# Kernel optimization log

Hardware: AMD Instinct MI355X
Metric: run time of the kernel (lower is better)

The kernel has to match this reference:

```python
import jax, jax.numpy as jnp
import numpy as np
import math

B, N, D = 2, 192, 256

def _linear_params(key, d_in, d_out):
    kw, kb = jax.random.split(key)
    scale = 1.0 / math.sqrt(d_in)
    W = jax.random.uniform(kw, (d_out, d_in), jnp.float32, -scale, scale)
    b = jax.random.uniform(kb, (d_out,), jnp.float32, -scale, scale)
    return W, b

def setup_inputs() -> dict:
    key = jax.random.key(0)
    ks = jax.random.split(key, 7)
    Edges = jax.random.normal(ks[0], (B, N * N, D), jnp.float32)
    Wq_w, Wq_b = _linear_params(ks[1], D, D)
    Wk_w, Wk_b = _linear_params(ks[2], D, D)
    Wv_w, Wv_b = _linear_params(ks[3], D, D)
    Wb_w, Wb_b = _linear_params(ks[4], D, 1)
    Wg_w, Wg_b = _linear_params(ks[5], D, D)
    Wo_w, Wo_b = _linear_params(ks[6], D, D)
    return {"Edges": Edges, "Wq_w": Wq_w, "Wq_b": Wq_b, "Wk_w": Wk_w, "Wk_b": Wk_b,
            "Wv_w": Wv_w, "Wv_b": Wv_b, "Wb_w": Wb_w, "Wb_b": Wb_b,
            "Wg_w": Wg_w, "Wg_b": Wg_b, "Wo_w": Wo_w, "Wo_b": Wo_b}

def reference(Edges, Wq_w, Wq_b, Wk_w, Wk_b, Wv_w, Wv_b, Wb_w, Wb_b, Wg_w, Wg_b, Wo_w, Wo_b):
    # Edges: [B, N*N, D]; dropout is identity in eval mode.
    Bb, NN, Dd = Edges.shape
    n = int(round(math.sqrt(NN)))
    q = (Edges @ Wq_w.T + Wq_b).reshape(Bb, n, n, Dd)
    k = (Edges @ Wk_w.T + Wk_b).reshape(Bb, n, n, Dd)
    v = (Edges @ Wv_w.T + Wv_b).reshape(Bb, n, n, Dd)
    bmat = (Edges @ Wb_w.T + Wb_b).reshape(Bb, n, n)          # b[b,i,l]
    g = jax.nn.sigmoid(Edges @ Wg_w.T + Wg_b)                  # [B, N*N, D]
    # row attention: q(i,j) . k(i,l) ; column attention: q(i,j) . k(l,j)
    scores = (jnp.einsum('bijd,bild->bijl', q, k)
              + jnp.einsum('bijd,bljd->bijl', q, k)) / math.sqrt(Dd)
    sym_bias = bmat + jnp.swapaxes(bmat, 1, 2)                 # b[i,l] + b[l,i]
    alpha = jax.nn.softmax(scores + sym_bias[:, :, None, :], axis=-1)  # [B,n,n,n]
    # first value contraction along rows; second term matches torch's
    # transpose-free add: out2[b,i,j,d] = sum_l alpha[b,j,i,l] v[b,l,i,d]
    o1 = jnp.einsum('bijl,bild->bijd', alpha, v)
    o2 = jnp.einsum('bjil,blid->bijd', alpha, v)
    out = g * (o1 + o2).reshape(Bb, NN, Dd)
    out = jax.nn.relu(out @ Wo_w.T + Wo_b)
    return out
```

## Files before the change

kernel.cpp:

```cpp
#include <hip/hip_runtime.h>
#include <hip/hip_bf16.h>

typedef __hip_bfloat16 bf16;
typedef unsigned short u16;
typedef __attribute__((ext_vector_type(8))) short bf16x8;
typedef __attribute__((ext_vector_type(4))) float f32x4;

#define NB   2
#define NG   192
#define DD   256
#define NN2  (NG*NG)
#define MT   (NB*NN2)

static __device__ __forceinline__ float bfu2f(u16 u){
    return __uint_as_float(((unsigned)u) << 16);
}
static __device__ __forceinline__ u16 f2bfu(float f){
    bf16 h = __float2bfloat16(f);
    return *(u16*)&h;
}

static __device__ __forceinline__ void gl_lds16(const void* g, void* l){
    __builtin_amdgcn_global_load_lds(
        (const __attribute__((address_space(1))) unsigned int*)g,
        (__attribute__((address_space(3))) unsigned int*)l, 16, 0, 0);
}
static __device__ __forceinline__ int swz3(int x){ return ((x ^ (x>>3)) & 7) << 3; }

__global__ __launch_bounds__(256) void k_cast_eb(
    const float* __restrict__ E, const float* __restrict__ Wb,
    const float* __restrict__ bb, u16* __restrict__ Eb, float* __restrict__ bm)
{
    const int t = threadIdx.x;
    size_t base = (size_t)blockIdx.x*2048 + t*8;
    float4 x = *(const float4*)(E+base);
    float4 y = *(const float4*)(E+base+4);
    ushort4 a; a.x=f2bfu(x.x); a.y=f2bfu(x.y); a.z=f2bfu(x.z); a.w=f2bfu(x.w);
    ushort4 b; b.x=f2bfu(y.x); b.y=f2bfu(y.y); b.z=f2bfu(y.z); b.w=f2bfu(y.w);
    *(ushort4*)(Eb+base)   = a;
    *(ushort4*)(Eb+base+4) = b;
    const int l32 = t & 31;
    float4 w0 = ((const float4*)Wb)[l32*2];
    float4 w1 = ((const float4*)Wb)[l32*2+1];
    float s = x.x*w0.x + x.y*w0.y + x.z*w0.z + x.w*w0.w
            + y.x*w1.x + y.y*w1.y + y.z*w1.z + y.w*w1.w;
    #pragma unroll
    for (int off=1; off<32; off<<=1) s += __shfl_xor(s, off);
    if (l32 == 0) bm[blockIdx.x*8 + (t>>5)] = s + bb[0];
}

__global__ __launch_bounds__(256) void k_cast_w(
    const float* __restrict__ Wq, const float* __restrict__ Wk,
    const float* __restrict__ Wv, const float* __restrict__ Wg,
    const float* __restrict__ Wo,
    const float* __restrict__ bq, const float* __restrict__ bk,
    const float* __restrict__ bv, const float* __restrict__ bg,
    u16* __restrict__ Wcat, u16* __restrict__ Wob, float* __restrict__ biascat)
{
    int e = blockIdx.x*256 + threadIdx.x;
    Wcat[e]          = f2bfu(Wq[e]);
    Wcat[65536 + e]  = f2bfu(Wk[e]);
    Wcat[131072 + e] = f2bfu(Wv[e]);
    Wcat[196608 + e] = f2bfu(Wg[e]);
    Wob[e]           = f2bfu(Wo[e]);
    if (e < 1024){
        int p = e>>8, r = e&255;
        const float* bp = p==0?bq : p==1?bk : p==2?bv : bg;
        biascat[e] = bp[r];
    }
}

__global__ __launch_bounds__(256) void k_bias_sym(
    const float* __restrict__ bm, float* __restrict__ biassym)
{
    int rem = blockIdx.x*256 + threadIdx.x;
    int b = blockIdx.y;
    int i = rem / NG, l = rem % NG;
    biassym[(size_t)b*NN2 + rem] = bm[(size_t)b*NN2 + rem] + bm[(size_t)b*NN2 + l*NG + i];
}

static __device__ __forceinline__ void gemm128_dbuf(
    const u16* __restrict__ A, const u16* __restrict__ B,
    u16* As, u16* Bs, f32x4 acc[4][4], int t)
{
    const int lane = t & 63, w = t >> 6;
    const int wm = (w>>1)*64, wn = (w&1)*64;
    int offA[4], offB[4];
    #pragma unroll
    for (int f=0; f<4; f++){
        int ra = wm + f*16 + (lane&15);
        offA[f] = ra*32 + (((lane>>4) ^ ((ra>>1)&3)) << 3);
        int rb = wn + f*16 + (lane&15);
        offB[f] = rb*32 + (((lane>>4) ^ ((rb>>1)&3)) << 3);
    }
    auto stage = [&](int buf, int k0){
        #pragma unroll
        for (int it=0; it<2; it++){
            int c = it*256 + t;
            int row = c >> 2;
            int ks  = (c&3) ^ ((row>>1)&3);
            gl_lds16(A + (size_t)row*DD + k0 + ks*8, As + buf*4096 + c*8);
            gl_lds16(B + (size_t)row*DD + k0 + ks*8, Bs + buf*4096 + c*8);
        }
    };
    stage(0, 0);
    for (int ks=0; ks<8; ks++){
        if (ks<7){
            stage((ks+1)&1, (ks+1)*32);
            asm volatile("s_waitcnt vmcnt(4)" ::: "memory");
        } else {
            asm volatile("s_waitcnt vmcnt(0)" ::: "memory");
        }
        __builtin_amdgcn_s_barrier();
        const u16* Ab = As + (ks&1)*4096;
        const u16* Bb = Bs + (ks&1)*4096;
        bf16x8 a[4], b[4];
        #pragma unroll
        for (int f=0; f<4; f++) a[f] = *(const bf16x8*)(Ab + offA[f]);
        #pragma unroll
        for (int f=0; f<4; f++) b[f] = *(const bf16x8*)(Bb + offB[f]);
        #pragma unroll
        for (int mf=0; mf<4; mf++)
            #pragma unroll
            for (int nf=0; nf<4; nf++)
                acc[mf][nf] = __builtin_amdgcn_mfma_f32_16x16x32_bf16(a[mf], b[nf], acc[mf][nf], 0, 0, 0);
        __builtin_amdgcn_s_barrier();
    }
}

__global__ __launch_bounds__(256) void k_proj_mfma(
    const u16* __restrict__ Eb, const u16* __restrict__ Wcat,
    const float* __restrict__ biascat,
    u16* __restrict__ qb, u16* __restrict__ kb,
    u16* __restrict__ vb, u16* __restrict__ gb)
{
    __shared__ u16 As[2*4096];
    __shared__ u16 Bs[2*4096];
    const int blk = blockIdx.x;
    const int xj = blk & 7, xi = blk >> 3;
    const int m0 = (xj*72 + (xi>>3)) * 128;
    const int n0 = (xi & 7) * 128;
    const int t = threadIdx.x, lane = t&63, w = t>>6;
    f32x4 acc[4][4];
    #pragma unroll
    for (int i=0;i<4;i++)
        #pragma unroll
        for (int j=0;j<4;j++) acc[i][j] = f32x4{0.f,0.f,0.f,0.f};
    gemm128_dbuf(Eb + (size_t)m0*DD, Wcat + (size_t)n0*DD, As, Bs, acc, t);

    const int p = n0 >> 8;
    u16* outp = p==0?qb : p==1?kb : p==2?vb : gb;
    const int wm = (w>>1)*64, wn = (w&1)*64;
    #pragma unroll
    for (int mf=0; mf<4; mf++){
        int m = m0 + wm + mf*16 + (lane>>4)*4;
        #pragma unroll
        for (int nf=0; nf<4; nf++){
            int gn = n0 + wn + nf*16 + (lane&15);
            float bias = biascat[gn];
            int col = gn & 255;
            #pragma unroll
            for (int r=0; r<4; r++){
                float v = acc[mf][nf][r] + bias;
                if (p==3) v = 1.0f/(1.0f+__expf(-v));
                outp[(size_t)(m+r)*DD + col] = f2bfu(v);
            }
        }
    }
}

__global__ __launch_bounds__(256) void k_final_mfma(
    const u16* __restrict__ hb, const u16* __restrict__ Wob,
    const float* __restrict__ bo, float* __restrict__ out)
{
    __shared__ u16 As[2*4096];
    __shared__ u16 Bs[2*4096];
    const int blk = blockIdx.x;
    const int xj = blk & 7, xi = blk >> 3;
    const int m0 = (xj*72 + (xi>>1)) * 128;
    const int n0 = (xi & 1) * 128;
    const int t = threadIdx.x, lane = t&63, w = t>>6;
    f32x4 acc[4][4];
    #pragma unroll
    for (int i=0;i<4;i++)
        #pragma unroll
        for (int j=0;j<4;j++) acc[i][j] = f32x4{0.f,0.f,0.f,0.f};
    gemm128_dbuf(hb + (size_t)m0*DD, Wob + (size_t)n0*DD, As, Bs, acc, t);

    const int wm = (w>>1)*64, wn = (w&1)*64;
    #pragma unroll
    for (int mf=0; mf<4; mf++){
        int m = m0 + wm + mf*16 + (lane>>4)*4;
        #pragma unroll
        for (int nf=0; nf<4; nf++){
            int n = n0 + wn + nf*16 + (lane&15);
            float bias = bo[n];
            #pragma unroll
            for (int r=0; r<4; r++)
                out[(size_t)(m+r)*DD + n] = fmaxf(acc[mf][nf][r] + bias, 0.0f);
        }
    }
}

__global__ __launch_bounds__(512, 2) void k_scores(
    const u16* __restrict__ q, const u16* __restrict__ kmat,
    u16* __restrict__ S1, u16* __restrict__ S2T)
{
    __shared__ u16 As[2][NG*64];
    __shared__ u16 Bs[2][NG*64];
    const int MODE = blockIdx.y;
    const int z = blockIdx.x, b = z/NG, r = z%NG;
    const int t = threadIdx.x, lane = t&63, w = t>>6;
    const int wm = (w&3)*48, wn = (w>>2)*96;
    const size_t astr = MODE ? (size_t)NG*DD : (size_t)DD;
    const u16* Ab = MODE ? q    + ((size_t)b*NN2 + r)*DD : q    + ((size_t)b*NG + r)*NG*DD;
    const u16* Bb = MODE ? kmat + ((size_t)b*NN2 + r)*DD : kmat + ((size_t)b*NG + r)*NG*DD;

    f32x4 acc[3][6];
    #pragma unroll
    for (int i=0;i<3;i++)
        #pragma unroll
        for (int j=0;j<6;j++) acc[i][j] = f32x4{0.f,0.f,0.f,0.f};

    int offA[3], offB[6];
    #pragma unroll
    for (int mf=0; mf<3; mf++){
        int x = wm + mf*16 + (lane&15);
        offA[mf] = x*64 + (((lane>>4)<<3) ^ swz3(x));
    }
    #pragma unroll
    for (int nf=0; nf<6; nf++){
        int x = wn + nf*16 + (lane&15);
        offB[nf] = x*64 + (((lane>>4)<<3) ^ swz3(x));
    }

    auto stage = [&](int buf, int k0){
        #pragma unroll
        for (int rr=0; rr<3; rr++){
            int c = t + rr*512;
            int x = c>>3, l8e = (c&7)<<3;
            size_t ro = (size_t)x*astr + k0;
            gl_lds16(Ab + ro + (l8e ^ swz3(x)), &As[buf][c*8]);
            gl_lds16(Bb + ro + (l8e ^ swz3(x)), &Bs[buf][c*8]);
        }
    };

    stage(0, 0);
    for (int ks=0; ks<4; ks++){
        if (ks<3){
            stage((ks+1)&1, (ks+1)*64);
            asm volatile("s_waitcnt vmcnt(6)" ::: "memory");
        } else {
            asm volatile("s_waitcnt vmcnt(0)" ::: "memory");
        }
        __builtin_amdgcn_s_barrier();
        const u16* A = &As[ks&1][0];
        const u16* B = &Bs[ks&1][0];
        #pragma unroll
        for (int kk=0; kk<2; kk++){
            bf16x8 a[3];
            #pragma unroll
            for (int mf=0; mf<3; mf++) a[mf] = *(const bf16x8*)(A + (offA[mf]^(kk<<5)));
            #pragma unroll
            for (int nf=0; nf<6; nf++){
                bf16x8 bf = *(const bf16x8*)(B + (offB[nf]^(kk<<5)));
                #pragma unroll
                for (int mf=0; mf<3; mf++)
                    acc[mf][nf] = __builtin_amdgcn_mfma_f32_16x16x32_bf16(a[mf], bf, acc[mf][nf], 0, 0, 0);
            }
        }
        __builtin_amdgcn_s_barrier();
    }

    u16* outb = (MODE ? S2T : S1) + ((size_t)b*NG + r)*NN2;
    #pragma unroll
    for (int mf=0; mf<3; mf++){
        #pragma unroll
        for (int nf=0; nf<6; nf++){
            int lcol = wn + nf*16 + (lane&15);
            #pragma unroll
            for (int r4=0; r4<4; r4++){
                int x = wm + mf*16 + (lane>>4)*4 + r4;
                outb[(size_t)x*NG + lcol] = f2bfu(acc[mf][nf][r4]*0.0625f);
            }
        }
    }
}

__global__ __launch_bounds__(256) void k_softmax(
    const u16* __restrict__ S1, const u16* __restrict__ S2T,
    const float* __restrict__ biassym,
    u16* __restrict__ alpha, u16* __restrict__ alphaT)
{
    int rr   = blockIdx.x*4 + (threadIdx.x >> 6);
    int lane = threadIdx.x & 63;
    int b = blockIdx.y;
    int i = rr / NG, j = rr % NG;
    const u16* r1 = S1  + ((size_t)b*NN2 + rr)*NG;
    const u16* r2 = S2T + ((size_t)b*NN2 + (size_t)j*NG + i)*NG;
    const float* bs = biassym + ((size_t)b*NG + i)*NG;
    float vals[3];
    float mx = -1e30f;
    #pragma unroll
    for (int tt=0; tt<3; tt++){
        int l = lane + tt*64;
        float s = bfu2f(r1[l]) + bfu2f(r2[l]) + bs[l];
        vals[tt] = s;
        mx = fmaxf(mx, s);
    }
    #pragma unroll
    for (int off=32; off; off>>=1) mx = fmaxf(mx, __shfl_xor(mx, off));
    float sum = 0.f;
    #pragma unroll
    for (int tt=0; tt<3; tt++){ vals[tt] = __expf(vals[tt]-mx); sum += vals[tt]; }
    #pragma unroll
    for (int off=32; off; off>>=1) sum += __shfl_xor(sum, off);
    float inv = 1.0f/sum;
    u16* arow1 = alpha  + ((size_t)b*NN2 + rr)*NG;
    u16* arow2 = alphaT + ((size_t)b*NN2 + (size_t)j*NG + i)*NG;
    #pragma unroll
    for (int tt=0; tt<3; tt++){
        u16 vq = f2bfu(vals[tt]*inv);
        arow1[lane + tt*64] = vq;
        arow2[lane + tt*64] = vq;
    }
}

__global__ __launch_bounds__(512, 4) void k_attnout(
    const u16* __restrict__ alpha, const u16* __restrict__ alphaT,
    const u16* __restrict__ vb, const u16* __restrict__ gb, u16* __restrict__ hb)
{
    __shared__ u16 AsL[2][NG*64];
    __shared__ u16 Vs[128*64];
    const int z = blockIdx.x;
    const int xcd = z & 7, s = z >> 3;
    const int bi = xcd*48 + (s>>1), dh = s & 1;
    const int b = bi/NG, i = bi%NG;
    const int dbase = dh*128;
    const int t = threadIdx.x, lane = t&63, w = t>>6;
    const int wm = (w&1)*96, wn = (w>>1)*32;

    const u16* Abase0 = alpha  + (size_t)bi*NN2;
    const u16* Abase1 = alphaT + (size_t)bi*NN2;
    const u16* V0 = vb + (size_t)bi*NG*DD + dbase;
    const u16* V1 = vb + ((size_t)b*NG*NG + i)*DD + dbase;

    f32x4 acc[6][2];
    #pragma unroll
    for (int m=0;m<6;m++)
        #pragma unroll
        for (int n=0;n<2;n++) acc[m][n] = f32x4{0.f,0.f,0.f,0.f};

    int offA[6], offB[2];
    #pragma unroll
    for (int mf=0; mf<6; mf++){
        int j = wm + mf*16 + (lane&15);
        offA[mf] = j*64 + (((lane>>4)<<3) ^ swz3(j));
    }
    #pragma unroll
    for (int nf=0; nf<2; nf++){
        int d = wn + nf*16 + (lane&15);
        offB[nf] = d*64 + (((lane>>4)<<3) ^ swz3(d));
    }

    int4 vr[2];
    auto stageA = [&](int u, int buf){
        const u16* Ab = (u>=3) ? Abase1 : Abase0;
        int ls = (u>=3 ? u-3 : u)*64;
        #pragma unroll
        for (int rr=0; rr<3; rr++){
            int c = t + rr*512;
            int j = c>>3, l8e = (c&7)<<3;
            gl_lds16(Ab + (size_t)j*NG + ls + (l8e ^ swz3(j)), &AsL[buf][c*8]);
        }
    };
    auto loadV = [&](int u){
        int p = (u>=3), ls = (u>=3 ? u-3 : u)*64;
        #pragma unroll
        for (int rr=0; rr<2; rr++){
            int c = t + rr*512;
            int l = ls + (c>>4), d0 = (c&15)*8;
            const u16* src = p ? (V1 + (size_t)l*NG*DD + d0) : (V0 + (size_t)l*DD + d0);
            vr[rr] = *(const int4*)src;
        }
    };

    stageA(0, 0);
    loadV(0);
    for (int u=0; u<6; u++){
        #pragma unroll
        for (int rr=0; rr<2; rr++){
            int c = t + rr*512;
            int l = c>>4;
            l &= 63;
            int d0 = (c&15)*8, c3 = c&7;
            ushort* vp = (ushort*)&vr[rr];
            #pragma unroll
            for (int qd=0; qd<8; qd++)
                Vs[(d0+qd)*64 + (l ^ ((qd^c3)<<3))] = vp[qd];
        }
        if (u<5){ stageA(u+1, (u+1)&1); loadV(u+1); }
        asm volatile("s_waitcnt lgkmcnt(0)" ::: "memory");
        __builtin_amdgcn_s_barrier();
        const u16* A = &AsL[u&1][0];
        #pragma unroll
        for (int kk=0; kk<2; kk++){
            bf16x8 bfr[2];
            #pragma unroll
            for (int nf=0; nf<2; nf++) bfr[nf] = *(const bf16x8*)(Vs + (offB[nf]^(kk<<5)));
            #pragma unroll
            for (int mf=0; mf<6; mf++){
                bf16x8 afr = *(const bf16x8*)(A + (offA[mf]^(kk<<5)));
                acc[mf][0] = __builtin_amdgcn_mfma_f32_16x16x32_bf16(afr, bfr[0], acc[mf][0], 0, 0, 0);
                acc[mf][1] = __builtin_amdgcn_mfma_f32_16x16x32_bf16(afr, bfr[1], acc[mf][1], 0, 0, 0);
            }
        }
        __builtin_amdgcn_s_barrier();
    }

    #pragma unroll
    for (int mf=0; mf<6; mf++){
        #pragma unroll
        for (int nf=0; nf<2; nf++){
            #pragma unroll
            for (int r4=0; r4<4; r4++){
                int j = wm + mf*16 + (lane>>4)*4 + r4;
                int d = dbase + wn + nf*16 + (lane&15);
                size_t idx = ((size_t)bi*NG + j)*DD + d;
                hb[idx] = f2bfu(bfu2f(gb[idx]) * acc[mf][nf][r4]);
            }
        }
    }
}

extern "C" void kernel_launch(void* const* d_in, const int* in_sizes, int n_in,
                              void* d_out, int out_size, void* d_ws, size_t ws_size,
                              hipStream_t stream)
{
    const float* E  = (const float*)d_in[0];
    const float* Wq = (const float*)d_in[1];  const float* bq = (const float*)d_in[2];
    const float* Wk = (const float*)d_in[3];  const float* bk = (const float*)d_in[4];
    const float* Wv = (const float*)d_in[5];  const float* bv = (const float*)d_in[6];
    const float* Wb = (const float*)d_in[7];  const float* bb = (const float*)d_in[8];
    const float* Wg = (const float*)d_in[9];  const float* bg = (const float*)d_in[10];
    const float* Wo = (const float*)d_in[11]; const float* bo = (const float*)d_in[12];
    float* out = (float*)d_out;

    const size_t BF = (size_t)MT*DD*2;
    const size_t SC = (size_t)NB*NG*NG*NG*4;
    char* ws = (char*)d_ws;
    u16* Eb  = (u16*)ws;
    u16* S1  = (u16*)ws;
    u16* S2T = (u16*)(ws + SC/2);
    u16* hb  = (u16*)ws;
    u16* qb = (u16*)(ws + SC);           u16* alpha  = qb;
    u16* kb = (u16*)(ws + SC + BF);      u16* alphaT = kb;
    u16* vb = (u16*)(ws + SC + 2*BF);
    u16* gb = (u16*)(ws + SC + 3*BF);
    size_t tail = SC + 4*BF;
    float* bm      = (float*)(ws + tail); tail += (size_t)MT*4;
    float* biassym = (float*)(ws + tail); tail += (size_t)MT*4;
    u16* Wcat      = (u16*)(ws + tail);   tail += (size_t)1024*DD*2;
    u16* Wob       = (u16*)(ws + tail);   tail += (size_t)DD*DD*2;
    float* biascat = (float*)(ws + tail); tail += 1024*4;
    (void)ws_size;

    k_cast_w   <<<dim3(256), 256, 0, stream>>>(Wq,Wk,Wv,Wg,Wo, bq,bk,bv,bg, Wcat, Wob, biascat);
    k_cast_eb  <<<dim3(9216), 256, 0, stream>>>(E, Wb, bb, Eb, bm);
    k_proj_mfma<<<dim3(4608), 256, 0, stream>>>(Eb, Wcat, biascat, qb, kb, vb, gb);
    k_bias_sym <<<dim3(NN2/256, NB), 256, 0, stream>>>(bm, biassym);
    k_scores   <<<dim3(NB*NG, 2), 512, 0, stream>>>(qb, kb, S1, S2T);
    k_softmax  <<<dim3(NN2/4, NB), 256, 0, stream>>>(S1, S2T, biassym, alpha, alphaT);
    k_attnout  <<<dim3(NB*NG*2), 512, 0, stream>>>(alpha, alphaT, vb, gb, hb);
    k_final_mfma<<<dim3(1152), 256, 0, stream>>>(hb, Wob, bo, out);
}
```

Measured before the change: 227.6 us.

## Hold projection weight fragments in registers and stream only activations through LDS

The projection GEMM now preloads each wave's full 64x256 slice of the concatenated weight matrix into registers before the main loop, instead of staging weight tiles through shared memory each k-step. Only the activation tile is double-buffered through LDS, which halves LDS traffic and shared memory use. Launch bounds also request two blocks per CU. The cost is a large register footprint (32 bf16x8 fragments per lane), which may cause spilling or limit occupancy despite the hint.

```diff
diff --git a/kernel.cpp b/kernel.cpp
--- a/kernel.cpp
+++ b/kernel.cpp
@@ -128,29 +128,79 @@
     }
 }
 
-__global__ __launch_bounds__(256) void k_proj_mfma(
+__global__ __launch_bounds__(256, 2) void k_proj_mfma(
     const u16* __restrict__ Eb, const u16* __restrict__ Wcat,
     const float* __restrict__ biascat,
     u16* __restrict__ qb, u16* __restrict__ kb,
     u16* __restrict__ vb, u16* __restrict__ gb)
 {
     __shared__ u16 As[2*4096];
-    __shared__ u16 Bs[2*4096];
     const int blk = blockIdx.x;
     const int xj = blk & 7, xi = blk >> 3;
     const int m0 = (xj*72 + (xi>>3)) * 128;
     const int n0 = (xi & 7) * 128;
     const int t = threadIdx.x, lane = t&63, w = t>>6;
+    const int wm = (w>>1)*64, wn = (w&1)*64;
+
+    bf16x8 bfr[8][4];
+    {
+        const u16* Wb0 = Wcat + (size_t)(n0 + wn + (lane&15))*DD + (lane>>4)*8;
+        #pragma unroll
+        for (int f=0; f<4; f++){
+            const u16* Wr = Wb0 + (size_t)f*16*DD;
+            #pragma unroll
+            for (int ks=0; ks<8; ks++)
+                bfr[ks][f] = *(const bf16x8*)(Wr + ks*32);
+        }
+    }
+
+    const u16* A = Eb + (size_t)m0*DD;
+    int offA[4];
+    #pragma unroll
+    for (int f=0; f<4; f++){
+        int ra = wm + f*16 + (lane&15);
+        offA[f] = ra*32 + (((lane>>4) ^ ((ra>>1)&3)) << 3);
+    }
+    auto stageA = [&](int buf, int k0){
+        #pragma unroll
+        for (int it=0; it<2; it++){
+            int c = it*256 + t;
+            int row = c >> 2;
+            int ks  = (c&3) ^ ((row>>1)&3);
+            gl_lds16(A + (size_t)row*DD + k0 + ks*8, As + buf*4096 + c*8);
+        }
+    };
+
     f32x4 acc[4][4];
     #pragma unroll
     for (int i=0;i<4;i++)
         #pragma unroll
         for (int j=0;j<4;j++) acc[i][j] = f32x4{0.f,0.f,0.f,0.f};
-    gemm128_dbuf(Eb + (size_t)m0*DD, Wcat + (size_t)n0*DD, As, Bs, acc, t);
+
+    stageA(0, 0);
+    #pragma unroll
+    for (int ks=0; ks<8; ks++){
+        if (ks<7){
+            stageA((ks+1)&1, (ks+1)*32);
+            asm volatile("s_waitcnt vmcnt(2)" ::: "memory");
+        } else {
+            asm volatile("s_waitcnt vmcnt(0)" ::: "memory");
+        }
+        __builtin_amdgcn_s_barrier();
+        const u16* Ab = As + (ks&1)*4096;
+        bf16x8 a[4];
+        #pragma unroll
+        for (int f=0; f<4; f++) a[f] = *(const bf16x8*)(Ab + offA[f]);
+        #pragma unroll
+        for (int mf=0; mf<4; mf++)
+            #pragma unroll
+            for (int nf=0; nf<4; nf++)
+                acc[mf][nf] = __builtin_amdgcn_mfma_f32_16x16x32_bf16(a[mf], bfr[ks][nf], acc[mf][nf], 0, 0, 0);
+        __builtin_amdgcn_s_barrier();
+    }
 
     const int p = n0 >> 8;
     u16* outp = p==0?qb : p==1?kb : p==2?vb : gb;
-    const int wm = (w>>1)*64, wn = (w&1)*64;
     #pragma unroll
     for (int mf=0; mf<4; mf++){
         int m = m0 + wm + mf*16 + (lane>>4)*4;
```

Result: slower. 275.4 us (+21.0%).

## Fuse symmetric bias into scores epilogue and drop transposed alpha copy

Applied to the files above, without the earlier changes.

Removes the separate symmetric-bias kernel and adds b[i,l]+b[l,i] directly in the S1 epilogue of the scores kernel. Softmax no longer reads a bias array and writes only one alpha tensor instead of two. The attention-output kernel reads the transposed operand from the same alpha buffer using a strided access (stride N*N), which saves a full alpha write but makes those loads less contiguous. Rounding the bias into bf16 together with the scores may slightly change precision.

```diff
diff --git a/kernel.cpp b/kernel.cpp
--- a/kernel.cpp
+++ b/kernel.cpp
@@ -70,15 +70,6 @@
     }
 }
 
-__global__ __launch_bounds__(256) void k_bias_sym(
-    const float* __restrict__ bm, float* __restrict__ biassym)
-{
-    int rem = blockIdx.x*256 + threadIdx.x;
-    int b = blockIdx.y;
-    int i = rem / NG, l = rem % NG;
-    biassym[(size_t)b*NN2 + rem] = bm[(size_t)b*NN2 + rem] + bm[(size_t)b*NN2 + l*NG + i];
-}
-
 static __device__ __forceinline__ void gemm128_dbuf(
     const u16* __restrict__ A, const u16* __restrict__ B,
     u16* As, u16* Bs, f32x4 acc[4][4], int t)
@@ -204,6 +195,7 @@
 
 __global__ __launch_bounds__(512, 2) void k_scores(
     const u16* __restrict__ q, const u16* __restrict__ kmat,
+    const float* __restrict__ bm,
     u16* __restrict__ S1, u16* __restrict__ S2T)
 {
     __shared__ u16 As[2][NG*64];
@@ -273,15 +265,17 @@
     }
 
     u16* outb = (MODE ? S2T : S1) + ((size_t)b*NG + r)*NN2;
+    const float* bmb = bm + (size_t)b*NN2;
     #pragma unroll
     for (int mf=0; mf<3; mf++){
         #pragma unroll
         for (int nf=0; nf<6; nf++){
             int lcol = wn + nf*16 + (lane&15);
+            float bias = MODE ? 0.f : (bmb[(size_t)r*NG + lcol] + bmb[(size_t)lcol*NG + r]);
             #pragma unroll
             for (int r4=0; r4<4; r4++){
                 int x = wm + mf*16 + (lane>>4)*4 + r4;
-                outb[(size_t)x*NG + lcol] = f2bfu(acc[mf][nf][r4]*0.0625f);
+                outb[(size_t)x*NG + lcol] = f2bfu(acc[mf][nf][r4]*0.0625f + bias);
             }
         }
     }
@@ -289,8 +283,7 @@
 
 __global__ __launch_bounds__(256) void k_softmax(
     const u16* __restrict__ S1, const u16* __restrict__ S2T,
-    const float* __restrict__ biassym,
-    u16* __restrict__ alpha, u16* __restrict__ alphaT)
+    u16* __restrict__ alpha)
 {
     int rr   = blockIdx.x*4 + (threadIdx.x >> 6);
     int lane = threadIdx.x & 63;
@@ -298,13 +291,12 @@
     int i = rr / NG, j = rr % NG;
     const u16* r1 = S1  + ((size_t)b*NN2 + rr)*NG;
     const u16* r2 = S2T + ((size_t)b*NN2 + (size_t)j*NG + i)*NG;
-    const float* bs = biassym + ((size_t)b*NG + i)*NG;
     float vals[3];
     float mx = -1e30f;
     #pragma unroll
     for (int tt=0; tt<3; tt++){
         int l = lane + tt*64;
-        float s = bfu2f(r1[l]) + bfu2f(r2[l]) + bs[l];
+        float s = bfu2f(r1[l]) + bfu2f(r2[l]);
         vals[tt] = s;
         mx = fmaxf(mx, s);
     }
@@ -316,18 +308,14 @@
     #pragma unroll
     for (int off=32; off; off>>=1) sum += __shfl_xor(sum, off);
     float inv = 1.0f/sum;
-    u16* arow1 = alpha  + ((size_t)b*NN2 + rr)*NG;
-    u16* arow2 = alphaT + ((size_t)b*NN2 + (size_t)j*NG + i)*NG;
-    #pragma unroll
-    for (int tt=0; tt<3; tt++){
-        u16 vq = f2bfu(vals[tt]*inv);
-        arow1[lane + tt*64] = vq;
-        arow2[lane + tt*64] = vq;
-    }
+    u16* arow1 = alpha + ((size_t)b*NN2 + rr)*NG;
+    #pragma unroll
+    for (int tt=0; tt<3; tt++)
+        arow1[lane + tt*64] = f2bfu(vals[tt]*inv);
 }
 
 __global__ __launch_bounds__(512, 4) void k_attnout(
-    const u16* __restrict__ alpha, const u16* __restrict__ alphaT,
+    const u16* __restrict__ alpha,
     const u16* __restrict__ vb, const u16* __restrict__ gb, u16* __restrict__ hb)
 {
     __shared__ u16 AsL[2][NG*64];
@@ -340,8 +328,8 @@
     const int t = threadIdx.x, lane = t&63, w = t>>6;
     const int wm = (w&1)*96, wn = (w>>1)*32;
 
-    const u16* Abase0 = alpha  + (size_t)bi*NN2;
-    const u16* Abase1 = alphaT + (size_t)bi*NN2;
+    const u16* Abase0 = alpha + (size_t)bi*NN2;
+    const u16* Abase1 = alpha + ((size_t)b*NN2 + i)*NG;
     const u16* V0 = vb + (size_t)bi*NG*DD + dbase;
     const u16* V1 = vb + ((size_t)b*NG*NG + i)*DD + dbase;
 
@@ -366,12 +354,13 @@
     int4 vr[2];
     auto stageA = [&](int u, int buf){
         const u16* Ab = (u>=3) ? Abase1 : Abase0;
+        const size_t astrd = (u>=3) ? (size_t)NN2 : (size_t)NG;
         int ls = (u>=3 ? u-3 : u)*64;
         #pragma unroll
         for (int rr=0; rr<3; rr++){
             int c = t + rr*512;
             int j = c>>3, l8e = (c&7)<<3;
-            gl_lds16(Ab + (size_t)j*NG + ls + (l8e ^ swz3(j)), &AsL[buf][c*8]);
+            gl_lds16(Ab + (size_t)j*astrd + ls + (l8e ^ swz3(j)), &AsL[buf][c*8]);
         }
     };
     auto loadV = [&](int u){
@@ -453,13 +442,12 @@
     u16* S1  = (u16*)ws;
     u16* S2T = (u16*)(ws + SC/2);
     u16* hb  = (u16*)ws;
-    u16* qb = (u16*)(ws + SC);           u16* alpha  = qb;
-    u16* kb = (u16*)(ws + SC + BF);      u16* alphaT = kb;
+    u16* qb = (u16*)(ws + SC);           u16* alpha = qb;
+    u16* kb = (u16*)(ws + SC + BF);
     u16* vb = (u16*)(ws + SC + 2*BF);
     u16* gb = (u16*)(ws + SC + 3*BF);
     size_t tail = SC + 4*BF;
     float* bm      = (float*)(ws + tail); tail += (size_t)MT*4;
-    float* biassym = (float*)(ws + tail); tail += (size_t)MT*4;
     u16* Wcat      = (u16*)(ws + tail);   tail += (size_t)1024*DD*2;
     u16* Wob       = (u16*)(ws + tail);   tail += (size_t)DD*DD*2;
     float* biascat = (float*)(ws + tail); tail += 1024*4;
@@ -468,9 +456,8 @@
     k_cast_w   <<<dim3(256), 256, 0, stream>>>(Wq,Wk,Wv,Wg,Wo, bq,bk,bv,bg, Wcat, Wob, biascat);
     k_cast_eb  <<<dim3(9216), 256, 0, stream>>>(E, Wb, bb, Eb, bm);
     k_proj_mfma<<<dim3(4608), 256, 0, stream>>>(Eb, Wcat, biascat, qb, kb, vb, gb);
-    k_bias_sym <<<dim3(NN2/256, NB), 256, 0, stream>>>(bm, biassym);
-    k_scores   <<<dim3(NB*NG, 2), 512, 0, stream>>>(qb, kb, S1, S2T);
-    k_softmax  <<<dim3(NN2/4, NB), 256, 0, stream>>>(S1, S2T, biassym, alpha, alphaT);
-    k_attnout  <<<dim3(NB*NG*2), 512, 0, stream>>>(alpha, alphaT, vb, gb, hb);
+    k_scores   <<<dim3(NB*NG, 2), 512, 0, stream>>>(qb, kb, bm, S1, S2T);
+    k_softmax  <<<dim3(NN2/4, NB), 256, 0, stream>>>(S1, S2T, alpha);
+    k_attnout  <<<dim3(NB*NG*2), 512, 0, stream>>>(alpha, vb, gb, hb);
     k_final_mfma<<<dim3(1152), 256, 0, stream>>>(hb, Wob, bo, out);
 }
```

After: 223.0 us, median of 3. -2.0%, faster.
